# Kernel optimization log

Measured on AMD Instinct MI355X. Metric: run time of the kernel, lower is better.

Reference implementation:

```python
import jax, jax.numpy as jnp
import numpy as np

E, TOPK = 8, 2
N_EMBD, TEXT_DIM, FULL = 1024, 1024, 1024
BS, SEQ = 8, 512

def setup_inputs() -> dict:
    key = jax.random.key(0)
    ks = jax.random.split(key, 8)
    return {
        "x": jax.random.normal(ks[0], (BS, SEQ, N_EMBD), jnp.float32),
        "dec_embeddings": jax.random.normal(ks[1], (BS, TEXT_DIM), jnp.float32),
        # router is zero-init in the module, but use small random weights so top-k is non-degenerate
        "router_w": jax.random.normal(ks[2], (E, TEXT_DIM), jnp.float32) * 0.02,
        "router_b": jnp.zeros((E,), jnp.float32),
        "w1": jax.random.normal(ks[3], (E, N_EMBD, N_EMBD), jnp.float32) * 0.02,
        "w2": jax.random.normal(ks[4], (E, N_EMBD, FULL), jnp.float32) * 0.02,
        "b1": jnp.zeros((E, 1, N_EMBD), jnp.float32),
        "b2": jnp.zeros((E, 1, FULL), jnp.float32),
    }

def reference(x, dec_embeddings, router_w, router_b, w1, w2, b1, b2):
    bs, seqlen, n_embd = x.shape
    logits = dec_embeddings @ router_w.T + router_b          # (bs, E)
    gate_probs = jax.nn.softmax(logits, axis=-1)
    topk_w, topk_idx = jax.lax.top_k(gate_probs, TOPK)       # (bs, k)
    topk_w = topk_w / jnp.sum(topk_w, axis=-1, keepdims=True)
    # dense all-expert 2-layer MLP (as written in the original)
    hidden = jax.nn.relu(jnp.einsum('bsn,enh->ebsh', x, w1) + b1[:, None])   # (E,bs,S,H)
    out_all = jnp.einsum('ebsh,ehf->ebsf', hidden, w2) + b2[:, None]          # (E,bs,S,F)
    out_b = jnp.transpose(out_all, (1, 0, 2, 3))             # (bs,E,S,F)
    # gather top-k expert outputs per batch item and combine
    sel = jnp.take_along_axis(out_b, topk_idx[:, :, None, None], axis=1)      # (bs,k,S,F)
    final_output = jnp.sum(topk_w[:, :, None, None] * sel, axis=1)            # (bs,S,F)
    combined_mask = jnp.max(jax.nn.one_hot(topk_idx, E, dtype=x.dtype), axis=1)  # (bs,E)
    aux_loss = E * jnp.sum(jnp.mean(gate_probs, axis=0) * jnp.mean(combined_mask, axis=0))
    return final_output, aux_loss, combined_mask, logits
```

## Files before the change

### kernel.cpp

```cpp
#include <hip/hip_runtime.h>
#include <hip/hip_bf16.h>
#include <stdint.h>

#define EXP 8
#define DIM 1024
#define SEQL 512
#define BATCH 8
#define OUT_FINAL_N (BATCH * SEQL * DIM)
#define OFF_AUX    4194304
#define OFF_MASK   4194305
#define OFF_LOGITS 4194369

typedef __bf16 bf16_t;
typedef bf16_t bf16x8 __attribute__((ext_vector_type(8)));
typedef bf16_t bf16x4 __attribute__((ext_vector_type(4)));
typedef float  f32x4  __attribute__((ext_vector_type(4)));

typedef __attribute__((address_space(1))) void* as1p;
typedef __attribute__((address_space(3))) void* as3p;

__device__ __forceinline__ void glds16(const void* g, void* l) {
  __builtin_amdgcn_global_load_lds((as1p)(void*)g, (as3p)l, 16, 0, 0);
}

__global__ __launch_bounds__(256) void prep_kernel(
    const float* __restrict__ x, const float* __restrict__ dec,
    const float* __restrict__ rw, const float* __restrict__ rb,
    const float* __restrict__ w1, const float* __restrict__ w2,
    bf16_t* __restrict__ xb, bf16_t* __restrict__ w1t, bf16_t* __restrict__ w2t,
    float* __restrict__ out_aux, float* __restrict__ out_mask,
    float* __restrict__ out_logits, int* __restrict__ idx_ws,
    float* __restrict__ w_ws) {
  __shared__ __align__(16) char tileb[9216];
  __shared__ float part[256];
  __shared__ float lg64[64];
  __shared__ float probs[64];
  __shared__ float msk[64];
  const int bid = blockIdx.x;
  const int t = threadIdx.x;

  if (bid < 2048) {
    const int z = bid >> 8;
    const int rem = bid & 255;
    const int k0 = (rem >> 4) * 64;
    const int n0 = (rem & 15) * 64;
    const float* src = w1 + (size_t)z * DIM * DIM;
    bf16_t* dst = w1t + (size_t)z * DIM * DIM;
    const int c4 = t & 15;
    const int rr = t >> 4;
    float4 v[4];
#pragma unroll
    for (int r = 0; r < 4; ++r)
      v[r] = *(const float4*)(src + (size_t)(k0 + rr * 4 + r) * DIM + n0 + c4 * 4);
    const float* vp = (const float*)v;
#pragma unroll
    for (int c = 0; c < 4; ++c) {
      bf16x4 o;
#pragma unroll
      for (int jk = 0; jk < 4; ++jk) o[jk] = (bf16_t)vp[jk * 4 + c];
      *(bf16x4*)(tileb + (c4 * 4 + c) * 144 + rr * 8) = o;
    }
    __syncthreads();
#pragma unroll
    for (int ii = 0; ii < 2; ++ii) {
      const int n = (t >> 3) + 32 * ii;
      const int j = t & 7;
      bf16x8 vv = *(const bf16x8*)(tileb + n * 144 + j * 16);
      *(bf16x8*)(dst + (size_t)(n0 + n) * DIM + k0 + j * 8) = vv;
    }
  } else if (bid < 2048 + 512) {
    const int i0 = (bid - 2048) * 2048 + t;
    float4 v[8];
#pragma unroll
    for (int i = 0; i < 8; ++i) v[i] = ((const float4*)x)[i0 + i * 256];
#pragma unroll
    for (int i = 0; i < 8; ++i) {
      bf16x4 o;
      o[0] = (bf16_t)v[i].x; o[1] = (bf16_t)v[i].y;
      o[2] = (bf16_t)v[i].z; o[3] = (bf16_t)v[i].w;
      ((bf16x4*)xb)[i0 + i * 256] = o;
    }
  } else {
    const int p = t >> 2, seg = t & 3;
    const int b = p >> 3, e = p & 7;
    const float4* dv = (const float4*)(dec + b * DIM + seg * 256);
    const float4* wv = (const float4*)(rw + e * DIM + seg * 256);
    float s = 0.f;
#pragma unroll 8
    for (int i = 0; i < 64; ++i) {
      float4 a = dv[i], c = wv[i];
      s += a.x * c.x + a.y * c.y + a.z * c.z + a.w * c.w;
    }
    part[t] = s;
    __syncthreads();
    if (seg == 0) {
      float l = part[t] + part[t + 1] + part[t + 2] + part[t + 3] + rb[e];
      lg64[p] = l;
      out_logits[p] = l;
    }
    __syncthreads();
    if (t < 8) {
      float l[8];
      float mx = -1e30f;
#pragma unroll
      for (int k = 0; k < 8; ++k) { l[k] = lg64[t * 8 + k]; mx = fmaxf(mx, l[k]); }
      float pe[8];
      float sum = 0.f;
#pragma unroll
      for (int k = 0; k < 8; ++k) { pe[k] = expf(l[k] - mx); sum += pe[k]; }
      float inv = 1.f / sum;
#pragma unroll
      for (int k = 0; k < 8; ++k) { pe[k] *= inv; probs[t * 8 + k] = pe[k]; }
      int i0 = 0;
#pragma unroll
      for (int k = 1; k < 8; ++k) if (pe[k] > pe[i0]) i0 = k;
      int i1 = (i0 == 0) ? 1 : 0;
#pragma unroll
      for (int k = 0; k < 8; ++k) if (k != i0 && pe[k] > pe[i1]) i1 = k;
      float p0 = pe[i0], p1 = pe[i1];
      float invs = 1.f / (p0 + p1);
      idx_ws[t * 2] = i0;
      idx_ws[t * 2 + 1] = i1;
      w_ws[t * 2] = p0 * invs;
      w_ws[t * 2 + 1] = p1 * invs;
#pragma unroll
      for (int k = 0; k < 8; ++k) {
        float m = (k == i0 || k == i1) ? 1.f : 0.f;
        msk[t * 8 + k] = m;
        out_mask[t * 8 + k] = m;
      }
    }
    __syncthreads();
    if (t == 0) {
      float aux = 0.f;
#pragma unroll
      for (int k = 0; k < 8; ++k) {
        float mp = 0.f, mm = 0.f;
#pragma unroll
        for (int bb = 0; bb < 8; ++bb) { mp += probs[bb * 8 + k]; mm += msk[bb * 8 + k]; }
        aux += (mp * 0.125f) * (mm * 0.125f);
      }
      out_aux[0] = 8.f * aux;
    }
  }
}

__global__ __launch_bounds__(512, 2) void gemm1_kernel(const bf16_t* __restrict__ xb,
                                                       const bf16_t* __restrict__ w1t,
                                                       const float* __restrict__ b1,
                                                       const int* __restrict__ topk_idx,
                                                       bf16_t* __restrict__ hidden,
                                                       const float* __restrict__ w2,
                                                       bf16_t* __restrict__ w2t) {
  __shared__ __align__(16) char smem[73728];
  const int bid = blockIdx.x;
  const int tid = threadIdx.x;

  if (bid >= 256) {
    const int half = tid >> 8;
    const int tt = tid & 255;
    char* tb = smem + half * 9216;
    const int tile = (bid - 256) * 2 + half;
    const int z = tile >> 8;
    const int rem = tile & 255;
    const int k0 = (rem >> 4) * 64;
    const int n0 = (rem & 15) * 64;
    const float* src = w2 + (size_t)z * DIM * DIM;
    bf16_t* dst = w2t + (size_t)z * DIM * DIM;
    const int c4 = tt & 15;
    const int rr = tt >> 4;
    float4 v[4];
#pragma unroll
    for (int r = 0; r < 4; ++r)
      v[r] = *(const float4*)(src + (size_t)(k0 + rr * 4 + r) * DIM + n0 + c4 * 4);
    const float* vp = (const float*)v;
#pragma unroll
    for (int c = 0; c < 4; ++c) {
      bf16x4 o;
#pragma unroll
      for (int jk = 0; jk < 4; ++jk) o[jk] = (bf16_t)vp[jk * 4 + c];
      *(bf16x4*)(tb + (c4 * 4 + c) * 144 + rr * 8) = o;
    }
    __syncthreads();
#pragma unroll
    for (int ii = 0; ii < 2; ++ii) {
      const int n = (tt >> 3) + 32 * ii;
      const int j = tt & 7;
      bf16x8 vv = *(const bf16x8*)(tb + n * 144 + j * 16);
      *(bf16x8*)(dst + (size_t)(n0 + n) * DIM + k0 + j * 8) = vv;
    }
    return;
  }

  const int bN = bid & 7, bM = (bid >> 3) & 3, b = bid >> 5;
  const int g = tid >> 8;
  const int t = tid & 255;
  const int slot = b * 2 + g;
  const int e = topk_idx[slot];

  const bf16_t* A  = xb + ((size_t)b * SEQL + bM * 128) * DIM;
  const bf16_t* Bt = w1t + ((size_t)e * DIM + bN * 128) * DIM;

  char* sA = smem;
  char* sB = smem + 24576 + g * 24576;

  const int rlA = tid >> 2, cpA = (tid & 3) ^ (rlA & 3);
  const bf16_t* gA = A + (size_t)rlA * DIM + cpA * 8;
  const int rlB = t >> 2, cpB = (t & 3) ^ (rlB & 3);
  const bf16_t* gB0 = Bt + (size_t)rlB * DIM + cpB * 8;
  const bf16_t* gB1 = gB0 + (size_t)64 * DIM;

  const int lane = tid & 63, wg = (tid >> 6) & 3;
  const int wr = wg >> 1, wc = wg & 1;
  const int m15 = lane & 15, q = lane >> 4;
  const char* ra[4];
  const char* rb[4];
#pragma unroll
  for (int i = 0; i < 4; ++i) {
    const int r = wr * 64 + i * 16 + m15;
    ra[i] = sA + r * 64 + ((q ^ (r & 3)) * 16);
    const int n = wc * 64 + i * 16 + m15;
    rb[i] = sB + n * 64 + ((q ^ (n & 3)) * 16);
  }

  f32x4 acc[4][4];
#pragma unroll
  for (int i = 0; i < 4; ++i)
#pragma unroll
    for (int j = 0; j < 4; ++j) acc[i][j] = {0.f, 0.f, 0.f, 0.f};

  glds16(gA, sA + tid * 16);
  glds16(gB0, sB + t * 16);
  glds16(gB1, sB + 4096 + t * 16);
  glds16(gA + 32, sA + 8192 + tid * 16);
  glds16(gB0 + 32, sB + 8192 + t * 16);
  glds16(gB1 + 32, sB + 8192 + 4096 + t * 16);

  int cur = 0;
  for (int kt = 0; kt < 32; ++kt) {
    if (kt < 31) {
      asm volatile("s_waitcnt vmcnt(3)" ::: "memory");
    } else {
      asm volatile("s_waitcnt vmcnt(0)" ::: "memory");
    }
    __builtin_amdgcn_s_barrier();
    asm volatile("" ::: "memory");
    if (kt < 30) {
      int nb = cur + 2; if (nb >= 3) nb -= 3;
      const int off = (kt + 2) * 32;
      glds16(gA + off, sA + nb * 8192 + tid * 16);
      glds16(gB0 + off, sB + nb * 8192 + t * 16);
      glds16(gB1 + off, sB + nb * 8192 + 4096 + t * 16);
    }
    bf16x8 af[4], bfr[4];
#pragma unroll
    for (int i = 0; i < 4; ++i) af[i] = *(const bf16x8*)(ra[i] + cur * 8192);
#pragma unroll
    for (int j = 0; j < 4; ++j) bfr[j] = *(const bf16x8*)(rb[j] + cur * 8192);
    __builtin_amdgcn_s_setprio(1);
#pragma unroll
    for (int i = 0; i < 4; ++i)
#pragma unroll
      for (int j = 0; j < 4; ++j)
        acc[i][j] = __builtin_amdgcn_mfma_f32_16x16x32_bf16(af[i], bfr[j], acc[i][j], 0, 0, 0);
    __builtin_amdgcn_s_setprio(0);
    cur += 1; if (cur == 3) cur = 0;
  }

  __syncthreads();
  bf16_t* hb = (bf16_t*)(smem + g * 34816);
  const float* be = b1 + e * DIM;
#pragma unroll
  for (int i = 0; i < 4; ++i)
#pragma unroll
    for (int j = 0; j < 4; ++j) {
      const int colL = wc * 64 + j * 16 + m15;
      const float bias = be[bN * 128 + colL];
#pragma unroll
      for (int r = 0; r < 4; ++r) {
        const int rowL = wr * 64 + i * 16 + q * 4 + r;
        hb[rowL * 136 + colL] = (bf16_t)fmaxf(acc[i][j][r] + bias, 0.f);
      }
    }
  __syncthreads();
  bf16_t* H = hidden + (size_t)slot * SEQL * DIM + ((size_t)bM * 128) * DIM + bN * 128;
#pragma unroll
  for (int ii = 0; ii < 8; ++ii) {
    const int r = (t >> 4) + 16 * ii;
    const int c = t & 15;
    bf16x8 vv = *(const bf16x8*)(hb + r * 136 + c * 8);
    *(bf16x8*)(H + (size_t)r * DIM + c * 8) = vv;
  }
}

__global__ __launch_bounds__(512, 2) void gemm2_kernel(const bf16_t* __restrict__ hidden,
                                                       const bf16_t* __restrict__ w2t,
                                                       const float* __restrict__ b2,
                                                       const int* __restrict__ topk_idx,
                                                       const float* __restrict__ topk_w,
                                                       float* __restrict__ out) {
  __shared__ __align__(16) char smem[98304];
  const int tid = threadIdx.x;
  const int g = tid >> 8;
  const int t = tid & 255;
  const int bN = blockIdx.x, bM = blockIdx.y, b = blockIdx.z;
  const int slot = b * 2 + g;
  const int e = topk_idx[slot];
  const float sg = topk_w[slot];

  const bf16_t* A  = hidden + ((size_t)slot * SEQL + bM * 128) * DIM;
  const bf16_t* Bt = w2t + ((size_t)e * DIM + bN * 128) * DIM;

  char* sA = smem + g * 49152;
  char* sB = sA + 24576;

  const int rl = t >> 2, cp = (t & 3) ^ (rl & 3);
  const bf16_t* gA0 = A + (size_t)rl * DIM + cp * 8;
  const bf16_t* gA1 = gA0 + (size_t)64 * DIM;
  const bf16_t* gB0 = Bt + (size_t)rl * DIM + cp * 8;
  const bf16_t* gB1 = gB0 + (size_t)64 * DIM;

  const int lane = tid & 63, wg = (tid >> 6) & 3;
  const int wr = wg >> 1, wc = wg & 1;
  const int m15 = lane & 15, q = lane >> 4;
  const char* ra[4];
  const char* rb[4];
#pragma unroll
  for (int i = 0; i < 4; ++i) {
    const int r = wr * 64 + i * 16 + m15;
    ra[i] = sA + r * 64 + ((q ^ (r & 3)) * 16);
    const int n = wc * 64 + i * 16 + m15;
    rb[i] = sB + n * 64 + ((q ^ (n & 3)) * 16);
  }

  f32x4 acc[4][4];
#pragma unroll
  for (int i = 0; i < 4; ++i)
#pragma unroll
    for (int j = 0; j < 4; ++j) acc[i][j] = {0.f, 0.f, 0.f, 0.f};

  glds16(gA0, sA + t * 16);
  glds16(gA1, sA + 4096 + t * 16);
  glds16(gB0, sB + t * 16);
  glds16(gB1, sB + 4096 + t * 16);
  glds16(gA0 + 32, sA + 8192 + t * 16);
  glds16(gA1 + 32, sA + 8192 + 4096 + t * 16);
  glds16(gB0 + 32, sB + 8192 + t * 16);
  glds16(gB1 + 32, sB + 8192 + 4096 + t * 16);

  int cur = 0;
  for (int kt = 0; kt < 32; ++kt) {
    if (kt < 31) {
      asm volatile("s_waitcnt vmcnt(4)" ::: "memory");
    } else {
      asm volatile("s_waitcnt vmcnt(0)" ::: "memory");
    }
    __builtin_amdgcn_s_barrier();
    asm volatile("" ::: "memory");
    if (kt < 30) {
      int nb = cur + 2; if (nb >= 3) nb -= 3;
      const int off = (kt + 2) * 32;
      char* dA = sA + nb * 8192 + t * 16;
      char* dB = sB + nb * 8192 + t * 16;
      glds16(gA0 + off, dA);
      glds16(gA1 + off, dA + 4096);
      glds16(gB0 + off, dB);
      glds16(gB1 + off, dB + 4096);
    }
    bf16x8 af[4], bfr[4];
#pragma unroll
    for (int i = 0; i < 4; ++i) af[i] = *(const bf16x8*)(ra[i] + cur * 8192);
#pragma unroll
    for (int j = 0; j < 4; ++j) bfr[j] = *(const bf16x8*)(rb[j] + cur * 8192);
    __builtin_amdgcn_s_setprio(1);
#pragma unroll
    for (int i = 0; i < 4; ++i)
#pragma unroll
      for (int j = 0; j < 4; ++j)
        acc[i][j] = __builtin_amdgcn_mfma_f32_16x16x32_bf16(af[i], bfr[j], acc[i][j], 0, 0, 0);
    __builtin_amdgcn_s_setprio(0);
    cur += 1; if (cur == 3) cur = 0;
  }

  __syncthreads();
  float* scr = (float*)smem;
  const float w0 = topk_w[b * 2], w1v = topk_w[b * 2 + 1];
  const float* be0 = b2 + topk_idx[b * 2] * DIM;
  const float* be1 = b2 + topk_idx[b * 2 + 1] * DIM;
  float* O = out + (size_t)b * SEQL * DIM;
#pragma unroll
  for (int i = 0; i < 4; ++i) {
    if (g == 1) {
#pragma unroll
      for (int j = 0; j < 4; ++j)
#pragma unroll
        for (int r = 0; r < 4; ++r)
          scr[(j * 4 + r) * 256 + t] = sg * acc[i][j][r];
    }
    __syncthreads();
    if (g == 0) {
#pragma unroll
      for (int j = 0; j < 4; ++j) {
        const int col = bN * 128 + wc * 64 + j * 16 + m15;
        const float bb = w0 * be0[col] + w1v * be1[col];
        const int row = bM * 128 + wr * 64 + i * 16 + q * 4;
#pragma unroll
        for (int r = 0; r < 4; ++r)
          O[(size_t)(row + r) * DIM + col] =
              sg * acc[i][j][r] + scr[(j * 4 + r) * 256 + t] + bb;
      }
    }
    __syncthreads();
  }
}

extern "C" void kernel_launch(void* const* d_in, const int* in_sizes, int n_in,
                              void* d_out, int out_size, void* d_ws, size_t ws_size,
                              hipStream_t stream) {
  const float* x   = (const float*)d_in[0];
  const float* dec = (const float*)d_in[1];
  const float* rw  = (const float*)d_in[2];
  const float* rb  = (const float*)d_in[3];
  const float* w1  = (const float*)d_in[4];
  const float* w2  = (const float*)d_in[5];
  const float* b1  = (const float*)d_in[6];
  const float* b2  = (const float*)d_in[7];
  float* out = (float*)d_out;

  char* ws = (char*)d_ws;
  bf16_t* xb   = (bf16_t*)(ws);
  bf16_t* w1t  = (bf16_t*)(ws + (8u << 20));
  bf16_t* w2t  = (bf16_t*)(ws + (24u << 20));
  bf16_t* hid  = (bf16_t*)(ws + (40u << 20));
  int*    idxw = (int*)(ws + (56u << 20));
  float*  ww   = (float*)(ws + (56u << 20) + 64);

  hipLaunchKernelGGL(prep_kernel, dim3(2048 + 512 + 1), dim3(256), 0, stream,
                     x, dec, rw, rb, w1, w2, xb, w1t, w2t,
                     out + OFF_AUX, out + OFF_MASK, out + OFF_LOGITS, idxw, ww);
  hipLaunchKernelGGL(gemm1_kernel, dim3(256 + 1024), dim3(512), 0, stream,
                     xb, w1t, b1, idxw, hid, w2, w2t);
  hipLaunchKernelGGL(gemm2_kernel, dim3(8, 4, 8), dim3(512), 0, stream,
                     hid, w2t, b2, idxw, ww, out);
}
```

Measured before the change: 196.5 us.

## Deepen GEMM pipelines to four LDS stages and split gemm1 into per-slot blocks

Both GEMM kernels move from a 3-buffer to a 4-buffer LDS ring with three K-tiles in flight, to hide more global-load latency behind MFMA work. gemm1 is restructured from 512-thread blocks, where two expert slots shared one A tile, into 256-thread blocks that each handle one slot. This doubles the block count and loads A twice but shrinks LDS per block. The transpose blocks now process two tiles each with 256 threads. gemm2 LDS grows to 128KB per block, which may limit occupancy to one block per CU.

New measurement: 198.6 us. No clear change (+1.0%).

```diff
diff --git a/kernel.cpp b/kernel.cpp
--- a/kernel.cpp
+++ b/kernel.cpp
@@ -145,73 +145,75 @@
   }
 }
 
-__global__ __launch_bounds__(512, 2) void gemm1_kernel(const bf16_t* __restrict__ xb,
+__global__ __launch_bounds__(256, 2) void gemm1_kernel(const bf16_t* __restrict__ xb,
                                                        const bf16_t* __restrict__ w1t,
                                                        const float* __restrict__ b1,
                                                        const int* __restrict__ topk_idx,
                                                        bf16_t* __restrict__ hidden,
                                                        const float* __restrict__ w2,
                                                        bf16_t* __restrict__ w2t) {
-  __shared__ __align__(16) char smem[73728];
+  __shared__ __align__(16) char smem[65536];
   const int bid = blockIdx.x;
   const int tid = threadIdx.x;
 
-  if (bid >= 256) {
-    const int half = tid >> 8;
-    const int tt = tid & 255;
-    char* tb = smem + half * 9216;
-    const int tile = (bid - 256) * 2 + half;
-    const int z = tile >> 8;
-    const int rem = tile & 255;
-    const int k0 = (rem >> 4) * 64;
-    const int n0 = (rem & 15) * 64;
-    const float* src = w2 + (size_t)z * DIM * DIM;
-    bf16_t* dst = w2t + (size_t)z * DIM * DIM;
-    const int c4 = tt & 15;
-    const int rr = tt >> 4;
-    float4 v[4];
-#pragma unroll
-    for (int r = 0; r < 4; ++r)
-      v[r] = *(const float4*)(src + (size_t)(k0 + rr * 4 + r) * DIM + n0 + c4 * 4);
-    const float* vp = (const float*)v;
-#pragma unroll
-    for (int c = 0; c < 4; ++c) {
-      bf16x4 o;
-#pragma unroll
-      for (int jk = 0; jk < 4; ++jk) o[jk] = (bf16_t)vp[jk * 4 + c];
-      *(bf16x4*)(tb + (c4 * 4 + c) * 144 + rr * 8) = o;
-    }
-    __syncthreads();
-#pragma unroll
-    for (int ii = 0; ii < 2; ++ii) {
-      const int n = (tt >> 3) + 32 * ii;
-      const int j = tt & 7;
-      bf16x8 vv = *(const bf16x8*)(tb + n * 144 + j * 16);
-      *(bf16x8*)(dst + (size_t)(n0 + n) * DIM + k0 + j * 8) = vv;
+  if (bid >= 512) {
+    char* tb = smem;
+    const int base = (bid - 512) * 2;
+#pragma unroll
+    for (int it = 0; it < 2; ++it) {
+      const int tile = base + it;
+      const int z = tile >> 8;
+      const int rem = tile & 255;
+      const int k0 = (rem >> 4) * 64;
+      const int n0 = (rem & 15) * 64;
+      const float* src = w2 + (size_t)z * DIM * DIM;
+      bf16_t* dst = w2t + (size_t)z * DIM * DIM;
+      const int c4 = tid & 15;
+      const int rr = tid >> 4;
+      float4 v[4];
+#pragma unroll
+      for (int r = 0; r < 4; ++r)
+        v[r] = *(const float4*)(src + (size_t)(k0 + rr * 4 + r) * DIM + n0 + c4 * 4);
+      const float* vp = (const float*)v;
+#pragma unroll
+      for (int c = 0; c < 4; ++c) {
+        bf16x4 o;
+#pragma unroll
+        for (int jk = 0; jk < 4; ++jk) o[jk] = (bf16_t)vp[jk * 4 + c];
+        *(bf16x4*)(tb + (c4 * 4 + c) * 144 + rr * 8) = o;
+      }
+      __syncthreads();
+#pragma unroll
+      for (int ii = 0; ii < 2; ++ii) {
+        const int n = (tid >> 3) + 32 * ii;
+        const int j = tid & 7;
+        bf16x8 vv = *(const bf16x8*)(tb + n * 144 + j * 16);
+        *(bf16x8*)(dst + (size_t)(n0 + n) * DIM + k0 + j * 8) = vv;
+      }
+      __syncthreads();
     }
     return;
   }
 
-  const int bN = bid & 7, bM = (bid >> 3) & 3, b = bid >> 5;
-  const int g = tid >> 8;
-  const int t = tid & 255;
-  const int slot = b * 2 + g;
+  const int bN = bid & 7, bM = (bid >> 3) & 3, slot = bid >> 5;
+  const int t = tid;
+  const int b = slot >> 1;
   const int e = topk_idx[slot];
 
   const bf16_t* A  = xb + ((size_t)b * SEQL + bM * 128) * DIM;
   const bf16_t* Bt = w1t + ((size_t)e * DIM + bN * 128) * DIM;
 
   char* sA = smem;
-  char* sB = smem + 24576 + g * 24576;
-
-  const int rlA = tid >> 2, cpA = (tid & 3) ^ (rlA & 3);
-  const bf16_t* gA = A + (size_t)rlA * DIM + cpA * 8;
-  const int rlB = t >> 2, cpB = (t & 3) ^ (rlB & 3);
-  const bf16_t* gB0 = Bt + (size_t)rlB * DIM + cpB * 8;
-  const bf16_t* gB1 = gB0 + (size_t)64 * DIM;
-
-  const int lane = tid & 63, wg = (tid >> 6) & 3;
-  const int wr = wg >> 1, wc = wg & 1;
+  char* sB = smem + 32768;
+
+  const int rl = t >> 2, cp = (t & 3) ^ (rl & 3);
+  const bf16_t* ga0 = A + (size_t)rl * DIM + cp * 8;
+  const bf16_t* ga1 = ga0 + (size_t)64 * DIM;
+  const bf16_t* gb0 = Bt + (size_t)rl * DIM + cp * 8;
+  const bf16_t* gb1 = gb0 + (size_t)64 * DIM;
+
+  const int lane = t & 63, w = t >> 6;
+  const int wr = w >> 1, wc = w & 1;
   const int m15 = lane & 15, q = lane >> 4;
   const char* ra[4];
   const char* rb[4];
@@ -229,29 +231,32 @@
 #pragma unroll
     for (int j = 0; j < 4; ++j) acc[i][j] = {0.f, 0.f, 0.f, 0.f};
 
-  glds16(gA, sA + tid * 16);
-  glds16(gB0, sB + t * 16);
-  glds16(gB1, sB + 4096 + t * 16);
-  glds16(gA + 32, sA + 8192 + tid * 16);
-  glds16(gB0 + 32, sB + 8192 + t * 16);
-  glds16(gB1 + 32, sB + 8192 + 4096 + t * 16);
-
-  int cur = 0;
+  auto STAGE = [&](int kt, int nb) {
+    const int off = kt * 32;
+    glds16(ga0 + off, sA + nb * 8192 + t * 16);
+    glds16(ga1 + off, sA + nb * 8192 + 4096 + t * 16);
+    glds16(gb0 + off, sB + nb * 8192 + t * 16);
+    glds16(gb1 + off, sB + nb * 8192 + 4096 + t * 16);
+  };
+
+  STAGE(0, 0);
+  STAGE(1, 1);
+  STAGE(2, 2);
+
   for (int kt = 0; kt < 32; ++kt) {
-    if (kt < 31) {
-      asm volatile("s_waitcnt vmcnt(3)" ::: "memory");
+    if (kt < 30) {
+      asm volatile("s_waitcnt vmcnt(8)" ::: "memory");
+    } else if (kt == 30) {
+      asm volatile("s_waitcnt vmcnt(4)" ::: "memory");
     } else {
       asm volatile("s_waitcnt vmcnt(0)" ::: "memory");
     }
     __builtin_amdgcn_s_barrier();
     asm volatile("" ::: "memory");
-    if (kt < 30) {
-      int nb = cur + 2; if (nb >= 3) nb -= 3;
-      const int off = (kt + 2) * 32;
-      glds16(gA + off, sA + nb * 8192 + tid * 16);
-      glds16(gB0 + off, sB + nb * 8192 + t * 16);
-      glds16(gB1 + off, sB + nb * 8192 + 4096 + t * 16);
-    }
+    if (kt < 29) {
+      STAGE(kt + 3, (kt + 3) & 3);
+    }
+    const int cur = kt & 3;
     bf16x8 af[4], bfr[4];
 #pragma unroll
     for (int i = 0; i < 4; ++i) af[i] = *(const bf16x8*)(ra[i] + cur * 8192);
@@ -264,11 +269,10 @@
       for (int j = 0; j < 4; ++j)
         acc[i][j] = __builtin_amdgcn_mfma_f32_16x16x32_bf16(af[i], bfr[j], acc[i][j], 0, 0, 0);
     __builtin_amdgcn_s_setprio(0);
-    cur += 1; if (cur == 3) cur = 0;
   }
 
   __syncthreads();
-  bf16_t* hb = (bf16_t*)(smem + g * 34816);
+  bf16_t* hb = (bf16_t*)smem;
   const float* be = b1 + e * DIM;
 #pragma unroll
   for (int i = 0; i < 4; ++i)
@@ -299,7 +303,7 @@
                                                        const int* __restrict__ topk_idx,
                                                        const float* __restrict__ topk_w,
                                                        float* __restrict__ out) {
-  __shared__ __align__(16) char smem[98304];
+  __shared__ __align__(16) char smem[131072];
   const int tid = threadIdx.x;
   const int g = tid >> 8;
   const int t = tid & 255;
@@ -311,8 +315,8 @@
   const bf16_t* A  = hidden + ((size_t)slot * SEQL + bM * 128) * DIM;
   const bf16_t* Bt = w2t + ((size_t)e * DIM + bN * 128) * DIM;
 
-  char* sA = smem + g * 49152;
-  char* sB = sA + 24576;
+  char* sA = smem + g * 65536;
+  char* sB = sA + 32768;
 
   const int rl = t >> 2, cp = (t & 3) ^ (rl & 3);
   const bf16_t* gA0 = A + (size_t)rl * DIM + cp * 8;
@@ -339,34 +343,32 @@
 #pragma unroll
     for (int j = 0; j < 4; ++j) acc[i][j] = {0.f, 0.f, 0.f, 0.f};
 
-  glds16(gA0, sA + t * 16);
-  glds16(gA1, sA + 4096 + t * 16);
-  glds16(gB0, sB + t * 16);
-  glds16(gB1, sB + 4096 + t * 16);
-  glds16(gA0 + 32, sA + 8192 + t * 16);
-  glds16(gA1 + 32, sA + 8192 + 4096 + t * 16);
-  glds16(gB0 + 32, sB + 8192 + t * 16);
-  glds16(gB1 + 32, sB + 8192 + 4096 + t * 16);
-
-  int cur = 0;
+  auto STAGE = [&](int kt, int nb) {
+    const int off = kt * 32;
+    glds16(gA0 + off, sA + nb * 8192 + t * 16);
+    glds16(gA1 + off, sA + nb * 8192 + 4096 + t * 16);
+    glds16(gB0 + off, sB + nb * 8192 + t * 16);
+    glds16(gB1 + off, sB + nb * 8192 + 4096 + t * 16);
+  };
+
+  STAGE(0, 0);
+  STAGE(1, 1);
+  STAGE(2, 2);
+
   for (int kt = 0; kt < 32; ++kt) {
-    if (kt < 31) {
+    if (kt < 30) {
+      asm volatile("s_waitcnt vmcnt(8)" ::: "memory");
+    } else if (kt == 30) {
       asm volatile("s_waitcnt vmcnt(4)" ::: "memory");
     } else {
       asm volatile("s_waitcnt vmcnt(0)" ::: "memory");
     }
     __builtin_amdgcn_s_barrier();
     asm volatile("" ::: "memory");
-    if (kt < 30) {
-      int nb = cur + 2; if (nb >= 3) nb -= 3;
-      const int off = (kt + 2) * 32;
-      char* dA = sA + nb * 8192 + t * 16;
-      char* dB = sB + nb * 8192 + t * 16;
-      glds16(gA0 + off, dA);
-      glds16(gA1 + off, dA + 4096);
-      glds16(gB0 + off, dB);
-      glds16(gB1 + off, dB + 4096);
-    }
+    if (kt < 29) {
+      STAGE(kt + 3, (kt + 3) & 3);
+    }
+    const int cur = kt & 3;
     bf16x8 af[4], bfr[4];
 #pragma unroll
     for (int i = 0; i < 4; ++i) af[i] = *(const bf16x8*)(ra[i] + cur * 8192);
@@ -379,7 +381,6 @@
       for (int j = 0; j < 4; ++j)
         acc[i][j] = __builtin_amdgcn_mfma_f32_16x16x32_bf16(af[i], bfr[j], acc[i][j], 0, 0, 0);
     __builtin_amdgcn_s_setprio(0);
-    cur += 1; if (cur == 3) cur = 0;
   }
 
   __syncthreads();
@@ -438,7 +439,7 @@
   hipLaunchKernelGGL(prep_kernel, dim3(2048 + 512 + 1), dim3(256), 0, stream,
                      x, dec, rw, rb, w1, w2, xb, w1t, w2t,
                      out + OFF_AUX, out + OFF_MASK, out + OFF_LOGITS, idxw, ww);
-  hipLaunchKernelGGL(gemm1_kernel, dim3(256 + 1024), dim3(512), 0, stream,
+  hipLaunchKernelGGL(gemm1_kernel, dim3(512 + 1024), dim3(256), 0, stream,
                      xb, w1t, b1, idxw, hid, w2, w2t);
   hipLaunchKernelGGL(gemm2_kernel, dim3(8, 4, 8), dim3(512), 0, stream,
                      hid, w2t, b2, idxw, ww, out);
```

## Split gemm1 into per-slot 256-thread blocks and remap block order for XCD locality

Applied to the files above, without the earlier changes.

gemm1 blocks that previously computed both top-k expert slots while sharing the A tile now each handle a single slot with 256 threads. This halves LDS use per block and doubles the block count, at the cost of loading the x tile twice. The w2 transpose blocks now process two tiles sequentially with 256 threads. Both GEMMs remap the block index with a stride-8 swizzle, so neighbouring tiles of the same batch or expert land on the same XCD for better L2 reuse.

Measured after the change: 191.9 us. 1.02x faster.

```diff
diff --git a/kernel.cpp b/kernel.cpp
--- a/kernel.cpp
+++ b/kernel.cpp
@@ -145,73 +145,76 @@
   }
 }
 
-__global__ __launch_bounds__(512, 2) void gemm1_kernel(const bf16_t* __restrict__ xb,
+__global__ __launch_bounds__(256, 2) void gemm1_kernel(const bf16_t* __restrict__ xb,
                                                        const bf16_t* __restrict__ w1t,
                                                        const float* __restrict__ b1,
                                                        const int* __restrict__ topk_idx,
                                                        bf16_t* __restrict__ hidden,
                                                        const float* __restrict__ w2,
                                                        bf16_t* __restrict__ w2t) {
-  __shared__ __align__(16) char smem[73728];
+  __shared__ __align__(16) char smem[49152];
   const int bid = blockIdx.x;
   const int tid = threadIdx.x;
 
-  if (bid >= 256) {
-    const int half = tid >> 8;
-    const int tt = tid & 255;
-    char* tb = smem + half * 9216;
-    const int tile = (bid - 256) * 2 + half;
-    const int z = tile >> 8;
-    const int rem = tile & 255;
-    const int k0 = (rem >> 4) * 64;
-    const int n0 = (rem & 15) * 64;
-    const float* src = w2 + (size_t)z * DIM * DIM;
-    bf16_t* dst = w2t + (size_t)z * DIM * DIM;
-    const int c4 = tt & 15;
-    const int rr = tt >> 4;
-    float4 v[4];
-#pragma unroll
-    for (int r = 0; r < 4; ++r)
-      v[r] = *(const float4*)(src + (size_t)(k0 + rr * 4 + r) * DIM + n0 + c4 * 4);
-    const float* vp = (const float*)v;
-#pragma unroll
-    for (int c = 0; c < 4; ++c) {
-      bf16x4 o;
-#pragma unroll
-      for (int jk = 0; jk < 4; ++jk) o[jk] = (bf16_t)vp[jk * 4 + c];
-      *(bf16x4*)(tb + (c4 * 4 + c) * 144 + rr * 8) = o;
-    }
-    __syncthreads();
-#pragma unroll
-    for (int ii = 0; ii < 2; ++ii) {
-      const int n = (tt >> 3) + 32 * ii;
-      const int j = tt & 7;
-      bf16x8 vv = *(const bf16x8*)(tb + n * 144 + j * 16);
-      *(bf16x8*)(dst + (size_t)(n0 + n) * DIM + k0 + j * 8) = vv;
+  if (bid >= 512) {
+    char* tb = smem;
+    const int base = (bid - 512) * 2;
+#pragma unroll
+    for (int it = 0; it < 2; ++it) {
+      const int tile = base + it;
+      const int z = tile >> 8;
+      const int rem = tile & 255;
+      const int k0 = (rem >> 4) * 64;
+      const int n0 = (rem & 15) * 64;
+      const float* src = w2 + (size_t)z * DIM * DIM;
+      bf16_t* dst = w2t + (size_t)z * DIM * DIM;
+      const int c4 = tid & 15;
+      const int rr = tid >> 4;
+      float4 v[4];
+#pragma unroll
+      for (int r = 0; r < 4; ++r)
+        v[r] = *(const float4*)(src + (size_t)(k0 + rr * 4 + r) * DIM + n0 + c4 * 4);
+      const float* vp = (const float*)v;
+#pragma unroll
+      for (int c = 0; c < 4; ++c) {
+        bf16x4 o;
+#pragma unroll
+        for (int jk = 0; jk < 4; ++jk) o[jk] = (bf16_t)vp[jk * 4 + c];
+        *(bf16x4*)(tb + (c4 * 4 + c) * 144 + rr * 8) = o;
+      }
+      __syncthreads();
+#pragma unroll
+      for (int ii = 0; ii < 2; ++ii) {
+        const int n = (tid >> 3) + 32 * ii;
+        const int j = tid & 7;
+        bf16x8 vv = *(const bf16x8*)(tb + n * 144 + j * 16);
+        *(bf16x8*)(dst + (size_t)(n0 + n) * DIM + k0 + j * 8) = vv;
+      }
+      __syncthreads();
     }
     return;
   }
 
-  const int bN = bid & 7, bM = (bid >> 3) & 3, b = bid >> 5;
-  const int g = tid >> 8;
-  const int t = tid & 255;
-  const int slot = b * 2 + g;
+  const int wg = (bid & 7) * 64 + (bid >> 3);
+  const int bN = wg & 7, bM = (wg >> 3) & 3, slot = wg >> 5;
+  const int t = tid;
+  const int b = slot >> 1;
   const int e = topk_idx[slot];
 
   const bf16_t* A  = xb + ((size_t)b * SEQL + bM * 128) * DIM;
   const bf16_t* Bt = w1t + ((size_t)e * DIM + bN * 128) * DIM;
 
   char* sA = smem;
-  char* sB = smem + 24576 + g * 24576;
-
-  const int rlA = tid >> 2, cpA = (tid & 3) ^ (rlA & 3);
-  const bf16_t* gA = A + (size_t)rlA * DIM + cpA * 8;
-  const int rlB = t >> 2, cpB = (t & 3) ^ (rlB & 3);
-  const bf16_t* gB0 = Bt + (size_t)rlB * DIM + cpB * 8;
-  const bf16_t* gB1 = gB0 + (size_t)64 * DIM;
-
-  const int lane = tid & 63, wg = (tid >> 6) & 3;
-  const int wr = wg >> 1, wc = wg & 1;
+  char* sB = smem + 24576;
+
+  const int rl = t >> 2, cp = (t & 3) ^ (rl & 3);
+  const bf16_t* ga0 = A + (size_t)rl * DIM + cp * 8;
+  const bf16_t* ga1 = ga0 + (size_t)64 * DIM;
+  const bf16_t* gb0 = Bt + (size_t)rl * DIM + cp * 8;
+  const bf16_t* gb1 = gb0 + (size_t)64 * DIM;
+
+  const int lane = t & 63, w = t >> 6;
+  const int wr = w >> 1, wc = w & 1;
   const int m15 = lane & 15, q = lane >> 4;
   const char* ra[4];
   const char* rb[4];
@@ -229,17 +232,19 @@
 #pragma unroll
     for (int j = 0; j < 4; ++j) acc[i][j] = {0.f, 0.f, 0.f, 0.f};
 
-  glds16(gA, sA + tid * 16);
-  glds16(gB0, sB + t * 16);
-  glds16(gB1, sB + 4096 + t * 16);
-  glds16(gA + 32, sA + 8192 + tid * 16);
-  glds16(gB0 + 32, sB + 8192 + t * 16);
-  glds16(gB1 + 32, sB + 8192 + 4096 + t * 16);
+  glds16(ga0, sA + t * 16);
+  glds16(ga1, sA + 4096 + t * 16);
+  glds16(gb0, sB + t * 16);
+  glds16(gb1, sB + 4096 + t * 16);
+  glds16(ga0 + 32, sA + 8192 + t * 16);
+  glds16(ga1 + 32, sA + 8192 + 4096 + t * 16);
+  glds16(gb0 + 32, sB + 8192 + t * 16);
+  glds16(gb1 + 32, sB + 8192 + 4096 + t * 16);
 
   int cur = 0;
   for (int kt = 0; kt < 32; ++kt) {
     if (kt < 31) {
-      asm volatile("s_waitcnt vmcnt(3)" ::: "memory");
+      asm volatile("s_waitcnt vmcnt(4)" ::: "memory");
     } else {
       asm volatile("s_waitcnt vmcnt(0)" ::: "memory");
     }
@@ -248,9 +253,12 @@
     if (kt < 30) {
       int nb = cur + 2; if (nb >= 3) nb -= 3;
       const int off = (kt + 2) * 32;
-      glds16(gA + off, sA + nb * 8192 + tid * 16);
-      glds16(gB0 + off, sB + nb * 8192 + t * 16);
-      glds16(gB1 + off, sB + nb * 8192 + 4096 + t * 16);
+      char* dA = sA + nb * 8192 + t * 16;
+      char* dB = sB + nb * 8192 + t * 16;
+      glds16(ga0 + off, dA);
+      glds16(ga1 + off, dA + 4096);
+      glds16(gb0 + off, dB);
+      glds16(gb1 + off, dB + 4096);
     }
     bf16x8 af[4], bfr[4];
 #pragma unroll
@@ -268,7 +276,7 @@
   }
 
   __syncthreads();
-  bf16_t* hb = (bf16_t*)(smem + g * 34816);
+  bf16_t* hb = (bf16_t*)smem;
   const float* be = b1 + e * DIM;
 #pragma unroll
   for (int i = 0; i < 4; ++i)
@@ -303,7 +311,9 @@
   const int tid = threadIdx.x;
   const int g = tid >> 8;
   const int t = tid & 255;
-  const int bN = blockIdx.x, bM = blockIdx.y, b = blockIdx.z;
+  const int raw = blockIdx.x;
+  const int wg = (raw & 7) * 32 + (raw >> 3);
+  const int bN = wg & 7, bM = (wg >> 3) & 3, b = wg >> 5;
   const int slot = b * 2 + g;
   const int e = topk_idx[slot];
   const float sg = topk_w[slot];
@@ -320,8 +330,8 @@
   const bf16_t* gB0 = Bt + (size_t)rl * DIM + cp * 8;
   const bf16_t* gB1 = gB0 + (size_t)64 * DIM;
 
-  const int lane = tid & 63, wg = (tid >> 6) & 3;
-  const int wr = wg >> 1, wc = wg & 1;
+  const int lane = tid & 63, wgv = (tid >> 6) & 3;
+  const int wr = wgv >> 1, wc = wgv & 1;
   const int m15 = lane & 15, q = lane >> 4;
   const char* ra[4];
   const char* rb[4];
@@ -438,8 +448,8 @@
   hipLaunchKernelGGL(prep_kernel, dim3(2048 + 512 + 1), dim3(256), 0, stream,
                      x, dec, rw, rb, w1, w2, xb, w1t, w2t,
                      out + OFF_AUX, out + OFF_MASK, out + OFF_LOGITS, idxw, ww);
-  hipLaunchKernelGGL(gemm1_kernel, dim3(256 + 1024), dim3(512), 0, stream,
+  hipLaunchKernelGGL(gemm1_kernel, dim3(512 + 1024), dim3(256), 0, stream,
                      xb, w1t, b1, idxw, hid, w2, w2t);
-  hipLaunchKernelGGL(gemm2_kernel, dim3(8, 4, 8), dim3(512), 0, stream,
+  hipLaunchKernelGGL(gemm2_kernel, dim3(256), dim3(512), 0, stream,
                      hid, w2t, b2, idxw, ww, out);
 }
```

## Rewrite gemm1 as 256x256 tiles with 8-wave ping-pong pipeline and remap block ids

Applied to the files above, without the earlier changes.

The first expert GEMM now uses one 256x256 output tile per block, computed by 8 waves, instead of 128x128 tiles that shared an A tile across two expert slots. K is staged in 64-wide double-buffered chunks in 128 KB of LDS with an 8-way XOR swizzle, and MFMA quadrants are interleaved with barriers and async global-to-LDS loads in a ping-pong schedule. The epilogue writes out the result in two row chunks. Both GEMMs also remap block ids so that consecutive blocks land on different XCDs for better L2 locality. The larger tile raises data reuse per block but halves the GEMM block count and uses all of LDS, so each CU holds only one such block.

Measured after the change: 194.4 us. About the same (-1.1%).

```diff
diff --git a/kernel.cpp b/kernel.cpp
--- a/kernel.cpp
+++ b/kernel.cpp
@@ -145,6 +145,39 @@
   }
 }
 
+#define BARx() do { asm volatile("" ::: "memory"); __builtin_amdgcn_s_barrier(); asm volatile("" ::: "memory"); } while (0)
+
+#define STAGEA(d, h, kk) do { \
+  char* _dst = smem + ((d) * 2 + (h)) * 16384 + tid * 16; \
+  const bf16_t* _src = gA + (size_t)((h) * 128) * DIM + (kk) * 64; \
+  glds16(_src, _dst); glds16(_src + (size_t)64 * DIM, _dst + 8192); } while (0)
+
+#define STAGEB(d, h, kk) do { \
+  char* _dst = smem + 65536 + ((d) * 2 + (h)) * 16384 + tid * 16; \
+  const bf16_t* _src = gB + (size_t)((h) * 128) * DIM + (kk) * 64; \
+  glds16(_src, _dst); glds16(_src + (size_t)64 * DIM, _dst + 8192); } while (0)
+
+#define LOADA(d, mh) do { \
+  const char* _ba = smem + ((d) * 2 + wr) * 16384 + (mh) * 8192; \
+  _Pragma("unroll") for (int _il = 0; _il < 4; ++_il) { \
+    af[_il][0] = *(const bf16x8*)(_ba + _il * 2048 + abase0); \
+    af[_il][1] = *(const bf16x8*)(_ba + _il * 2048 + abase1); } } while (0)
+
+#define LOADB(d, nh) do { \
+  const char* _bb = smem + 65536 + ((d) * 2 + (wc >> 1)) * 16384; \
+  _Pragma("unroll") for (int _jl = 0; _jl < 2; ++_jl) { \
+    bfr[(nh) * 2 + _jl][0] = *(const bf16x8*)(_bb + ((nh) * 2 + _jl) * 2048 + bbase0); \
+    bfr[(nh) * 2 + _jl][1] = *(const bf16x8*)(_bb + ((nh) * 2 + _jl) * 2048 + bbase1); } } while (0)
+
+#define MMAQ(mh, nh) do { __builtin_amdgcn_s_setprio(1); \
+  _Pragma("unroll") for (int _il = 0; _il < 4; ++_il) \
+  _Pragma("unroll") for (int _jl = 0; _jl < 2; ++_jl) { \
+    acc[(mh) * 4 + _il][(nh) * 2 + _jl] = __builtin_amdgcn_mfma_f32_16x16x32_bf16( \
+        af[_il][0], bfr[(nh) * 2 + _jl][0], acc[(mh) * 4 + _il][(nh) * 2 + _jl], 0, 0, 0); \
+    acc[(mh) * 4 + _il][(nh) * 2 + _jl] = __builtin_amdgcn_mfma_f32_16x16x32_bf16( \
+        af[_il][1], bfr[(nh) * 2 + _jl][1], acc[(mh) * 4 + _il][(nh) * 2 + _jl], 0, 0, 0); } \
+  __builtin_amdgcn_s_setprio(0); } while (0)
+
 __global__ __launch_bounds__(512, 2) void gemm1_kernel(const bf16_t* __restrict__ xb,
                                                        const bf16_t* __restrict__ w1t,
                                                        const float* __restrict__ b1,
@@ -152,15 +185,15 @@
                                                        bf16_t* __restrict__ hidden,
                                                        const float* __restrict__ w2,
                                                        bf16_t* __restrict__ w2t) {
-  __shared__ __align__(16) char smem[73728];
+  __shared__ __align__(16) char smem[131072];
   const int bid = blockIdx.x;
   const int tid = threadIdx.x;
 
-  if (bid >= 256) {
+  if (bid >= 128) {
     const int half = tid >> 8;
     const int tt = tid & 255;
     char* tb = smem + half * 9216;
-    const int tile = (bid - 256) * 2 + half;
+    const int tile = (bid - 128) * 2 + half;
     const int z = tile >> 8;
     const int rem = tile & 255;
     const int k0 = (rem >> 4) * 64;
@@ -192,104 +225,98 @@
     return;
   }
 
-  const int bN = bid & 7, bM = (bid >> 3) & 3, b = bid >> 5;
-  const int g = tid >> 8;
-  const int t = tid & 255;
-  const int slot = b * 2 + g;
+  const int wgid = (bid & 7) * 16 + (bid >> 3);
+  const int bN = wgid & 3, bM = (wgid >> 2) & 1, slot = wgid >> 3;
+  const int b = slot >> 1;
   const int e = topk_idx[slot];
 
-  const bf16_t* A  = xb + ((size_t)b * SEQL + bM * 128) * DIM;
-  const bf16_t* Bt = w1t + ((size_t)e * DIM + bN * 128) * DIM;
-
-  char* sA = smem;
-  char* sB = smem + 24576 + g * 24576;
-
-  const int rlA = tid >> 2, cpA = (tid & 3) ^ (rlA & 3);
-  const bf16_t* gA = A + (size_t)rlA * DIM + cpA * 8;
-  const int rlB = t >> 2, cpB = (t & 3) ^ (rlB & 3);
-  const bf16_t* gB0 = Bt + (size_t)rlB * DIM + cpB * 8;
-  const bf16_t* gB1 = gB0 + (size_t)64 * DIM;
-
-  const int lane = tid & 63, wg = (tid >> 6) & 3;
-  const int wr = wg >> 1, wc = wg & 1;
+  const bf16_t* A  = xb + ((size_t)b * SEQL + bM * 256) * DIM;
+  const bf16_t* Bt = w1t + ((size_t)e * DIM + bN * 256) * DIM;
+
+  const int srow = tid >> 3;
+  const int sc = (tid & 7) ^ (srow & 7);
+  const bf16_t* gA = A + (size_t)srow * DIM + sc * 8;
+  const bf16_t* gB = Bt + (size_t)srow * DIM + sc * 8;
+
+  const int lane = tid & 63, w = tid >> 6;
+  const int wr = w >> 2, wc = w & 3;
   const int m15 = lane & 15, q = lane >> 4;
-  const char* ra[4];
-  const char* rb[4];
-#pragma unroll
-  for (int i = 0; i < 4; ++i) {
-    const int r = wr * 64 + i * 16 + m15;
-    ra[i] = sA + r * 64 + ((q ^ (r & 3)) * 16);
-    const int n = wc * 64 + i * 16 + m15;
-    rb[i] = sB + n * 64 + ((q ^ (n & 3)) * 16);
-  }
-
-  f32x4 acc[4][4];
-#pragma unroll
-  for (int i = 0; i < 4; ++i)
+  const int abase0 = m15 * 128 + ((q ^ (m15 & 7)) * 16);
+  const int abase1 = m15 * 128 + (((4 + q) ^ (m15 & 7)) * 16);
+  const int bbase0 = (wc & 1) * 8192 + abase0;
+  const int bbase1 = (wc & 1) * 8192 + abase1;
+
+  f32x4 acc[8][4];
+#pragma unroll
+  for (int i = 0; i < 8; ++i)
 #pragma unroll
     for (int j = 0; j < 4; ++j) acc[i][j] = {0.f, 0.f, 0.f, 0.f};
-
-  glds16(gA, sA + tid * 16);
-  glds16(gB0, sB + t * 16);
-  glds16(gB1, sB + 4096 + t * 16);
-  glds16(gA + 32, sA + 8192 + tid * 16);
-  glds16(gB0 + 32, sB + 8192 + t * 16);
-  glds16(gB1 + 32, sB + 8192 + 4096 + t * 16);
-
-  int cur = 0;
-  for (int kt = 0; kt < 32; ++kt) {
-    if (kt < 31) {
-      asm volatile("s_waitcnt vmcnt(3)" ::: "memory");
-    } else {
-      asm volatile("s_waitcnt vmcnt(0)" ::: "memory");
-    }
-    __builtin_amdgcn_s_barrier();
-    asm volatile("" ::: "memory");
-    if (kt < 30) {
-      int nb = cur + 2; if (nb >= 3) nb -= 3;
-      const int off = (kt + 2) * 32;
-      glds16(gA + off, sA + nb * 8192 + tid * 16);
-      glds16(gB0 + off, sB + nb * 8192 + t * 16);
-      glds16(gB1 + off, sB + nb * 8192 + 4096 + t * 16);
-    }
-    bf16x8 af[4], bfr[4];
-#pragma unroll
-    for (int i = 0; i < 4; ++i) af[i] = *(const bf16x8*)(ra[i] + cur * 8192);
-#pragma unroll
-    for (int j = 0; j < 4; ++j) bfr[j] = *(const bf16x8*)(rb[j] + cur * 8192);
-    __builtin_amdgcn_s_setprio(1);
-#pragma unroll
-    for (int i = 0; i < 4; ++i)
-#pragma unroll
-      for (int j = 0; j < 4; ++j)
-        acc[i][j] = __builtin_amdgcn_mfma_f32_16x16x32_bf16(af[i], bfr[j], acc[i][j], 0, 0, 0);
-    __builtin_amdgcn_s_setprio(0);
-    cur += 1; if (cur == 3) cur = 0;
-  }
-
-  __syncthreads();
-  bf16_t* hb = (bf16_t*)(smem + g * 34816);
+  bf16x8 af[4][2], bfr[4][2];
+
+  STAGEB(0, 0, 0); STAGEB(0, 1, 0); STAGEA(0, 0, 0); STAGEA(0, 1, 0);
+  STAGEB(1, 0, 1); STAGEB(1, 1, 1); STAGEA(1, 0, 1);
+  asm volatile("s_waitcnt vmcnt(6)" ::: "memory");
+  __builtin_amdgcn_s_barrier();
+  asm volatile("" ::: "memory");
+
+  for (int it = 0; it < 8; ++it) {
+    const int k1 = 2 * it + 1, k2 = 2 * it + 2, k3 = 2 * it + 3;
+    LOADA(0, 0); LOADB(0, 0);
+    STAGEA(1, 1, k1);
+    BARx(); MMAQ(0, 0); BARx();
+    LOADB(0, 1);
+    BARx(); MMAQ(0, 1); BARx();
+    LOADA(0, 1);
+    if (it < 7) STAGEB(0, 0, k2);
+    BARx(); MMAQ(1, 1); BARx();
+    if (it < 7) { STAGEB(0, 1, k2); STAGEA(0, 0, k2); }
+    BARx(); MMAQ(1, 0);
+    if (it < 7) { asm volatile("s_waitcnt vmcnt(6)" ::: "memory"); }
+    else        { asm volatile("s_waitcnt vmcnt(0)" ::: "memory"); }
+    BARx();
+    LOADA(1, 0); LOADB(1, 0);
+    if (it < 7) STAGEA(0, 1, k2);
+    BARx(); MMAQ(0, 0); BARx();
+    LOADB(1, 1);
+    BARx(); MMAQ(0, 1); BARx();
+    LOADA(1, 1);
+    if (it < 7) STAGEB(1, 0, k3);
+    BARx(); MMAQ(1, 1); BARx();
+    if (it < 7) { STAGEB(1, 1, k3); STAGEA(1, 0, k3); }
+    BARx(); MMAQ(1, 0);
+    if (it < 7) { asm volatile("s_waitcnt vmcnt(6)" ::: "memory"); }
+    BARx();
+  }
+
   const float* be = b1 + e * DIM;
 #pragma unroll
-  for (int i = 0; i < 4; ++i)
-#pragma unroll
-    for (int j = 0; j < 4; ++j) {
-      const int colL = wc * 64 + j * 16 + m15;
-      const float bias = be[bN * 128 + colL];
-#pragma unroll
-      for (int r = 0; r < 4; ++r) {
-        const int rowL = wr * 64 + i * 16 + q * 4 + r;
-        hb[rowL * 136 + colL] = (bf16_t)fmaxf(acc[i][j][r] + bias, 0.f);
-      }
-    }
-  __syncthreads();
-  bf16_t* H = hidden + (size_t)slot * SEQL * DIM + ((size_t)bM * 128) * DIM + bN * 128;
-#pragma unroll
-  for (int ii = 0; ii < 8; ++ii) {
-    const int r = (t >> 4) + 16 * ii;
-    const int c = t & 15;
-    bf16x8 vv = *(const bf16x8*)(hb + r * 136 + c * 8);
-    *(bf16x8*)(H + (size_t)r * DIM + c * 8) = vv;
+  for (int mchunk = 0; mchunk < 2; ++mchunk) {
+    __syncthreads();
+    bf16_t* hb = (bf16_t*)smem;
+    if (wr == mchunk) {
+#pragma unroll
+      for (int fi = 0; fi < 8; ++fi)
+#pragma unroll
+        for (int fj = 0; fj < 4; ++fj) {
+          const int colL = wc * 64 + fj * 16 + m15;
+          const float bias = be[bN * 256 + colL];
+#pragma unroll
+          for (int r = 0; r < 4; ++r) {
+            const int rowL = fi * 16 + q * 4 + r;
+            hb[rowL * 264 + colL] = (bf16_t)fmaxf(acc[fi][fj][r] + bias, 0.f);
+          }
+        }
+    }
+    __syncthreads();
+    bf16_t* H = hidden + (size_t)slot * SEQL * DIM +
+                (size_t)(bM * 256 + mchunk * 128) * DIM + bN * 256;
+#pragma unroll
+    for (int ii = 0; ii < 8; ++ii) {
+      const int rr_ = (tid >> 5) + ii * 16;
+      const int cc_ = (tid & 31) * 8;
+      bf16x8 vv = *(const bf16x8*)(hb + rr_ * 264 + cc_);
+      *(bf16x8*)(H + (size_t)rr_ * DIM + cc_) = vv;
+    }
   }
 }
 
@@ -299,11 +326,13 @@
                                                        const int* __restrict__ topk_idx,
                                                        const float* __restrict__ topk_w,
                                                        float* __restrict__ out) {
-  __shared__ __align__(16) char smem[98304];
+  __shared__ __align__(16) char smem2[98304];
   const int tid = threadIdx.x;
   const int g = tid >> 8;
   const int t = tid & 255;
-  const int bN = blockIdx.x, bM = blockIdx.y, b = blockIdx.z;
+  const int raw = blockIdx.x;
+  const int wg = (raw & 7) * 32 + (raw >> 3);
+  const int bN = wg & 7, bM = (wg >> 3) & 3, b = wg >> 5;
   const int slot = b * 2 + g;
   const int e = topk_idx[slot];
   const float sg = topk_w[slot];
@@ -311,7 +340,7 @@
   const bf16_t* A  = hidden + ((size_t)slot * SEQL + bM * 128) * DIM;
   const bf16_t* Bt = w2t + ((size_t)e * DIM + bN * 128) * DIM;
 
-  char* sA = smem + g * 49152;
+  char* sA = smem2 + g * 49152;
   char* sB = sA + 24576;
 
   const int rl = t >> 2, cp = (t & 3) ^ (rl & 3);
@@ -320,8 +349,8 @@
   const bf16_t* gB0 = Bt + (size_t)rl * DIM + cp * 8;
   const bf16_t* gB1 = gB0 + (size_t)64 * DIM;
 
-  const int lane = tid & 63, wg = (tid >> 6) & 3;
-  const int wr = wg >> 1, wc = wg & 1;
+  const int lane = tid & 63, wgv = (tid >> 6) & 3;
+  const int wr = wgv >> 1, wc = wgv & 1;
   const int m15 = lane & 15, q = lane >> 4;
   const char* ra[4];
   const char* rb[4];
@@ -367,23 +396,23 @@
       glds16(gB0 + off, dB);
       glds16(gB1 + off, dB + 4096);
     }
-    bf16x8 af[4], bfr[4];
-#pragma unroll
-    for (int i = 0; i < 4; ++i) af[i] = *(const bf16x8*)(ra[i] + cur * 8192);
-#pragma unroll
-    for (int j = 0; j < 4; ++j) bfr[j] = *(const bf16x8*)(rb[j] + cur * 8192);
+    bf16x8 af2[4], bfr2[4];
+#pragma unroll
+    for (int i = 0; i < 4; ++i) af2[i] = *(const bf16x8*)(ra[i] + cur * 8192);
+#pragma unroll
+    for (int j = 0; j < 4; ++j) bfr2[j] = *(const bf16x8*)(rb[j] + cur * 8192);
     __builtin_amdgcn_s_setprio(1);
 #pragma unroll
     for (int i = 0; i < 4; ++i)
 #pragma unroll
       for (int j = 0; j < 4; ++j)
-        acc[i][j] = __builtin_amdgcn_mfma_f32_16x16x32_bf16(af[i], bfr[j], acc[i][j], 0, 0, 0);
+        acc[i][j] = __builtin_amdgcn_mfma_f32_16x16x32_bf16(af2[i], bfr2[j], acc[i][j], 0, 0, 0);
     __builtin_amdgcn_s_setprio(0);
     cur += 1; if (cur == 3) cur = 0;
   }
 
   __syncthreads();
-  float* scr = (float*)smem;
+  float* scr = (float*)smem2;
   const float w0 = topk_w[b * 2], w1v = topk_w[b * 2 + 1];
   const float* be0 = b2 + topk_idx[b * 2] * DIM;
   const float* be1 = b2 + topk_idx[b * 2 + 1] * DIM;
@@ -438,8 +467,8 @@
   hipLaunchKernelGGL(prep_kernel, dim3(2048 + 512 + 1), dim3(256), 0, stream,
                      x, dec, rw, rb, w1, w2, xb, w1t, w2t,
                      out + OFF_AUX, out + OFF_MASK, out + OFF_LOGITS, idxw, ww);
-  hipLaunchKernelGGL(gemm1_kernel, dim3(256 + 1024), dim3(512), 0, stream,
+  hipLaunchKernelGGL(gemm1_kernel, dim3(128 + 1024), dim3(512), 0, stream,
                      xb, w1t, b1, idxw, hid, w2, w2t);
-  hipLaunchKernelGGL(gemm2_kernel, dim3(8, 4, 8), dim3(512), 0, stream,
+  hipLaunchKernelGGL(gemm2_kernel, dim3(256), dim3(512), 0, stream,
                      hid, w2t, b2, idxw, ww, out);
 }
```
